# Optimization experiments

Hardware: AMD Instinct MI355X
Metric: run time of the kernel (lower is better)

The kernel has to match this reference:

```python
import jax, jax.numpy as jnp
import numpy as np

B, N, D = 2, 2048, 1024          # batch, seq (= wh*ww), model dim
H, HD = 16, 64                   # heads, head_dim (inner_dim = H*HD = D)
MLP = 4096                       # SwiGLU hidden dim
WSY, WSX = 16, 32                # ws_y = wh//2, ws_x = ww//2  (wh=32, ww=64)
EPS = float(jnp.finfo(jnp.float32).eps)  # torch RMSNorm default eps


def setup_inputs() -> dict:
    key = jax.random.key(0)
    ks = jax.random.split(key, 8)
    return {
        "x": jax.random.normal(ks[0], (B, N, D), jnp.float32),
        "t": jax.random.normal(ks[1], (B,), jnp.float32),
        "dt": jax.random.normal(ks[2], (B, D), jnp.float32),
        "w_qkv": (jax.random.normal(ks[3], (3 * H * HD, D), jnp.float32) * 0.02),
        "w_o": (jax.random.normal(ks[4], (D, H * HD), jnp.float32) * 0.02),
        "w1": (jax.random.normal(ks[5], (2 * MLP, D), jnp.float32) * 0.02),
        "w2": (jax.random.normal(ks[6], (D, MLP), jnp.float32) * 0.02),
        "g_attn": jnp.ones((D,), jnp.float32),  # RMSNorm weight (attn)
        "g_ff": jnp.ones((D,), jnp.float32),    # RMSNorm weight (ffn)
    }


def _rms(x, g):
    return x * jax.lax.rsqrt(jnp.mean(x * x, axis=-1, keepdims=True) + EPS) * g


def _win(x):
    # 'b h (wc_y wc_x ws_y ws_x) d' -> 'b h (wc_y ws_y wc_x ws_x) d'
    b, h, n, d = x.shape
    return x.reshape(b, h, 2, 2, WSY, WSX, d).transpose(0, 1, 2, 4, 3, 5, 6).reshape(b, h, n, d)


def _unwin(x):
    # inverse of _win
    b, h, n, d = x.shape
    return x.reshape(b, h, 2, WSY, 2, WSX, d).transpose(0, 1, 2, 4, 3, 5, 6).reshape(b, h, n, d)


def reference(x, t, dt, w_qkv, w_o, w1, w2, g_attn, g_ff):
    # ---- SPAttention (pre-norm); all-to-all is identity on 1 device ----
    h = _rms(x, g_attn)
    qkv = h @ w_qkv.T                              # [B,N,3*H*HD]
    q, k, v = jnp.split(qkv, 3, axis=-1)
    as_heads = lambda z: z.reshape(B, N, H, HD).transpose(0, 2, 1, 3)  # b h n d
    q, k, v = _win(as_heads(q)), _win(as_heads(k)), _win(as_heads(v))
    # NOTE: the source computes RoPE2D(q), RoPE2D(k) but discards the result;
    # attention consumes the UNROTATED seq_gathered_q/k/v. Faithful: no rotation.
    scale = 1.0 / jnp.sqrt(jnp.float32(HD))        # SDPA default scale
    s = jnp.einsum('bhqd,bhkd->bhqk', q, k) * scale
    a = jax.nn.softmax(s, axis=-1)
    o = jnp.einsum('bhqk,bhkd->bhqd', a, v)
    o = _unwin(o).transpose(0, 2, 1, 3).reshape(B, N, H * HD)
    x = x + o @ w_o.T                               # residual
    # ---- SwiGLU FeedForward (pre-norm) + residual ----
    hf = _rms(x, g_ff)
    gate, up = jnp.split(hf @ w1.T, 2, axis=-1)
    return x + (jax.nn.silu(gate) * up) @ w2.T
```

## Files before the change

### kernel.cpp

```cpp
#include <hip/hip_runtime.h>
#include <cstdint>
#include <cstddef>

typedef __attribute__((ext_vector_type(8)))  __bf16 bf16x8;
typedef __attribute__((ext_vector_type(4)))  __bf16 bf16x4;
typedef __attribute__((ext_vector_type(4)))  float  f32x4;
typedef __attribute__((ext_vector_type(16))) float  f32x16;
typedef __attribute__((ext_vector_type(4)))  uint32_t u32x4;

#define MFMA_BF16(a, b, c) __builtin_amdgcn_mfma_f32_16x16x32_bf16((a), (b), (c), 0, 0, 0)
#define MFMA32(a, b, c)    __builtin_amdgcn_mfma_f32_32x32x16_bf16((a), (b), (c), 0, 0, 0)

__device__ __forceinline__ void gload_lds16(const __bf16* src, __bf16* lds_dst) {
    __builtin_amdgcn_global_load_lds(
        (const __attribute__((address_space(1))) void*)(const_cast<__bf16*>(src)),
        (__attribute__((address_space(3))) void*)(lds_dst), 16, 0, 0);
}

__device__ __forceinline__ uint32_t pack2(float a, float b) {
    uint16_t ua = __builtin_bit_cast(uint16_t, (__bf16)a);
    uint16_t ub = __builtin_bit_cast(uint16_t, (__bf16)b);
    return (uint32_t)ua | ((uint32_t)ub << 16);
}

__global__ __launch_bounds__(256) void cvt_kernel(const float* __restrict__ src,
                                                  __bf16* __restrict__ dst) {
    int i = blockIdx.x * 256 + threadIdx.x;
    float4 v = reinterpret_cast<const float4*>(src)[i];
    bf16x4 o;
    o[0] = (__bf16)v.x; o[1] = (__bf16)v.y; o[2] = (__bf16)v.z; o[3] = (__bf16)v.w;
    reinterpret_cast<bf16x4*>(dst)[i] = o;
}

__global__ __launch_bounds__(256) void rmsnorm_kernel(const float* __restrict__ x,
                                                      const float* __restrict__ g,
                                                      __bf16* __restrict__ out) {
    const int row = blockIdx.x;
    const int t = threadIdx.x;
    float4 v = reinterpret_cast<const float4*>(x + (size_t)row * 1024)[t];
    float ss = v.x * v.x + v.y * v.y + v.z * v.z + v.w * v.w;
#pragma unroll
    for (int m = 1; m < 64; m <<= 1) ss += __shfl_xor(ss, m);
    __shared__ float sred[4];
    if ((t & 63) == 0) sred[t >> 6] = ss;
    __syncthreads();
    float tot = sred[0] + sred[1] + sred[2] + sred[3];
    float rs = rsqrtf(tot * (1.0f / 1024.0f) + 1.1920928955078125e-07f);
    float4 gv = reinterpret_cast<const float4*>(g)[t];
    bf16x4 o;
    o[0] = (__bf16)(v.x * rs * gv.x);
    o[1] = (__bf16)(v.y * rs * gv.y);
    o[2] = (__bf16)(v.z * rs * gv.z);
    o[3] = (__bf16)(v.w * rs * gv.w);
    *reinterpret_cast<bf16x4*>(out + (size_t)row * 1024 + t * 4) = o;
}

template <int MODE>
__global__ __launch_bounds__(256) void gemm_nt(const __bf16* __restrict__ A, int lda,
                                               const __bf16* __restrict__ B, int ldb,
                                               __bf16* __restrict__ outb,
                                               float* __restrict__ outf,
                                               const float* __restrict__ resid,
                                               int K, int ldo) {
    __shared__ __attribute__((aligned(16))) __bf16 As[128 * 64];
    __shared__ __attribute__((aligned(16))) __bf16 Bs[128 * 64];
    const int t = threadIdx.x;
    const int lane = t & 63;
    const int wid = t >> 6;
    const int bm = blockIdx.x, bn = blockIdx.y;
    const int wm = (wid >> 1) * 64, wn = (wid & 1) * 64;
    f32x4 acc[4][4] = {};

    for (int kt = 0; kt < K; kt += 64) {
        __syncthreads();
#pragma unroll
        for (int i = 0; i < 4; ++i) {
            int L = i * 256 + t;
            int r = L >> 3, s = L & 7;
            int c = s ^ (r & 7);
            const __bf16* sa = A + (size_t)(bm * 128 + r) * lda + kt + c * 8;
            gload_lds16(sa, As + L * 8);
            int rb = bn * 128 + r;
            int srow = (MODE == 2) ? ((rb >> 1) + ((rb & 1) << 12)) : rb;
            const __bf16* sb = B + (size_t)srow * ldb + kt + c * 8;
            gload_lds16(sb, Bs + L * 8);
        }
        __syncthreads();
#pragma unroll
        for (int ks = 0; ks < 2; ++ks) {
            bf16x8 af[4], bfr[4];
#pragma unroll
            for (int mi = 0; mi < 4; ++mi) {
                int r = wm + mi * 16 + (lane & 15);
                int slot = (ks * 4 + (lane >> 4)) ^ (r & 7);
                af[mi] = *reinterpret_cast<const bf16x8*>(As + r * 64 + slot * 8);
            }
#pragma unroll
            for (int ni = 0; ni < 4; ++ni) {
                int r = wn + ni * 16 + (lane & 15);
                int slot = (ks * 4 + (lane >> 4)) ^ (r & 7);
                bfr[ni] = *reinterpret_cast<const bf16x8*>(Bs + r * 64 + slot * 8);
            }
#pragma unroll
            for (int mi = 0; mi < 4; ++mi)
#pragma unroll
                for (int ni = 0; ni < 4; ++ni)
                    acc[mi][ni] = MFMA_BF16(af[mi], bfr[ni], acc[mi][ni]);
        }
    }
    const int row0 = bm * 128 + wm + ((lane >> 4) << 2);
    const int col0 = bn * 128 + wn + (lane & 15);
#pragma unroll
    for (int mi = 0; mi < 4; ++mi)
#pragma unroll
        for (int ni = 0; ni < 4; ++ni)
#pragma unroll
            for (int r2 = 0; r2 < 4; ++r2) {
                int row = row0 + mi * 16 + r2;
                int col = col0 + ni * 16;
                float v = acc[mi][ni][r2];
                if (MODE == 0) {
                    outb[(size_t)row * ldo + col] = (__bf16)v;
                } else if (MODE == 1) {
                    size_t idx = (size_t)row * ldo + col;
                    outf[idx] = v + resid[idx];
                } else {
                    float pv = __shfl_xor(v, 1);
                    if (!(lane & 1)) {
                        float sg = v / (1.0f + __expf(-v));
                        outb[(size_t)row * ldo + (col >> 1)] = (__bf16)(sg * pv);
                    }
                }
            }
}

__global__ __launch_bounds__(256) void vtrans_kernel(const __bf16* __restrict__ qkv,
                                                     __bf16* __restrict__ vt) {
    __shared__ __bf16 T[64][68];
    const int t = threadIdx.x;
    const int bh = blockIdx.y, b = bh >> 4, h = bh & 15;
    const int n0 = blockIdx.x * 64;
    const __bf16* vp = qkv + (size_t)b * 2048 * 3072 + 2048 + h * 64;
#pragma unroll
    for (int i = 0; i < 2; ++i) {
        int r = i * 32 + (t >> 3), c = t & 7;
        bf16x8 v = *reinterpret_cast<const bf16x8*>(vp + (size_t)(n0 + r) * 3072 + c * 8);
#pragma unroll
        for (int j = 0; j < 8; ++j) T[c * 8 + j][r] = v[j];
    }
    __syncthreads();
#pragma unroll
    for (int i = 0; i < 2; ++i) {
        int hd = i * 32 + (t >> 3), c = t & 7;
        bf16x8 v;
#pragma unroll
        for (int j = 0; j < 8; ++j) v[j] = T[hd][c * 8 + j];
        *reinterpret_cast<bf16x8*>(vt + ((size_t)bh * 64 + hd) * 2048 + n0 + c * 8) = v;
    }
}

__global__ __launch_bounds__(256) void attn_kernel(const __bf16* __restrict__ qkv,
                                                   const __bf16* __restrict__ vt,
                                                   __bf16* __restrict__ o) {
    __shared__ __attribute__((aligned(16))) __bf16 Ks[2][64 * 64];
    __shared__ __attribute__((aligned(16))) __bf16 Vs[2][64 * 64];
    const int t = threadIdx.x;
    const int lane = t & 63;
    const int w = t >> 6;
    const int hi = lane >> 5;
    const int l31 = lane & 31;
    const int bh = blockIdx.y;
    const int b = bh >> 4, h = bh & 15;
    const __bf16* qp = qkv + (size_t)b * 2048 * 3072 + h * 64;
    const __bf16* kp = qp + 1024;
    const __bf16* vtp = vt + (size_t)bh * 64 * 2048;
    const int q0 = blockIdx.x * 128 + w * 32;

    const float SC = 0.18033688011112042f;
    bf16x8 qf[4];
#pragma unroll
    for (int s = 0; s < 4; ++s) {
        bf16x8 raw = *reinterpret_cast<const bf16x8*>(
            qp + (size_t)(q0 + l31) * 3072 + s * 16 + hi * 8);
        bf16x8 sc;
#pragma unroll
        for (int j = 0; j < 8; ++j) sc[j] = (__bf16)((float)raw[j] * SC);
        qf[s] = sc;
    }

    f32x16 oa[2] = {};
    float m_run = -INFINITY, l_run = 0.0f;

    auto stage = [&](int buf, int kt) {
#pragma unroll
        for (int i = 0; i < 2; ++i) {
            int L = i * 256 + t;
            int r = L >> 3, s = L & 7;
            int c = s ^ (r & 7);
            gload_lds16(kp + (size_t)(kt + r) * 3072 + c * 8, &Ks[buf][L * 8]);
            gload_lds16(vtp + (size_t)r * 2048 + kt + c * 8, &Vs[buf][L * 8]);
        }
    };
    stage(0, 0);
    __syncthreads();

    for (int kt = 0; kt < 2048; kt += 64) {
        const int buf = (kt >> 6) & 1;
        if (kt + 64 < 2048) stage(buf ^ 1, kt + 64);

        f32x16 st[2] = {};
#pragma unroll
        for (int s = 0; s < 4; ++s) {
#pragma unroll
            for (int mb = 0; mb < 2; ++mb) {
                int r = mb * 32 + l31;
                int sl = (s * 2 + hi) ^ (r & 7);
                bf16x8 kf = *reinterpret_cast<const bf16x8*>(&Ks[buf][r * 64 + sl * 8]);
                st[mb] = MFMA32(kf, qf[s], st[mb]);
            }
        }
        float mt = -INFINITY;
#pragma unroll
        for (int mb = 0; mb < 2; ++mb)
#pragma unroll
            for (int r = 0; r < 16; ++r) mt = fmaxf(mt, st[mb][r]);
        mt = fmaxf(mt, __shfl_xor(mt, 32));
        const float m_new = fmaxf(m_run, mt);
        const float alpha = exp2f(m_run - m_new);
        float ps = 0.0f;
#pragma unroll
        for (int mb = 0; mb < 2; ++mb)
#pragma unroll
            for (int r = 0; r < 16; ++r) {
                float p = exp2f(st[mb][r] - m_new);
                st[mb][r] = p;
                ps += p;
            }
        ps += __shfl_xor(ps, 32);
        l_run = l_run * alpha + ps;
        m_run = m_new;

#pragma unroll
        for (int r = 0; r < 16; ++r) {
            float av = __shfl(alpha, (r & 3) + 8 * (r >> 2) + 4 * hi);
            oa[0][r] *= av;
            oa[1][r] *= av;
        }

        uint32_t pk[16], qk[16];
#pragma unroll
        for (int mb = 0; mb < 2; ++mb)
#pragma unroll
            for (int i2 = 0; i2 < 8; ++i2)
                pk[mb * 8 + i2] = pack2(st[mb][2 * i2], st[mb][2 * i2 + 1]);
#pragma unroll
        for (int i2 = 0; i2 < 16; ++i2)
            qk[i2] = (uint32_t)__shfl_xor((int)pk[i2], 32);

#pragma unroll
        for (int s2 = 0; s2 < 4; ++s2) {
            int mb = s2 >> 1, sl2 = s2 & 1;
            u32x4 fv;
            if (hi == 0) {
                fv[0] = pk[mb * 8 + 4 * sl2 + 0]; fv[1] = pk[mb * 8 + 4 * sl2 + 1];
                fv[2] = qk[mb * 8 + 4 * sl2 + 0]; fv[3] = qk[mb * 8 + 4 * sl2 + 1];
            } else {
                fv[0] = qk[mb * 8 + 4 * sl2 + 2]; fv[1] = qk[mb * 8 + 4 * sl2 + 3];
                fv[2] = pk[mb * 8 + 4 * sl2 + 2]; fv[3] = pk[mb * 8 + 4 * sl2 + 3];
            }
            bf16x8 pa = __builtin_bit_cast(bf16x8, fv);
#pragma unroll
            for (int nb = 0; nb < 2; ++nb) {
                int rv = nb * 32 + l31;
                int sl = (s2 * 2 + hi) ^ (rv & 7);
                bf16x8 vf = *reinterpret_cast<const bf16x8*>(&Vs[buf][rv * 64 + sl * 8]);
                oa[nb] = MFMA32(pa, vf, oa[nb]);
            }
        }
        __syncthreads();
    }

#pragma unroll
    for (int r = 0; r < 16; ++r) {
        int crow = (r & 3) + 8 * (r >> 2) + 4 * hi;
        float lv = __shfl(l_run, crow);
        float inv = 1.0f / lv;
        int row = q0 + crow;
        size_t base = ((size_t)b * 2048 + row) * 1024 + h * 64 + l31;
        o[base]      = (__bf16)(oa[0][r] * inv);
        o[base + 32] = (__bf16)(oa[1][r] * inv);
    }
}

extern "C" void kernel_launch(void* const* d_in, const int* in_sizes, int n_in,
                              void* d_out, int out_size, void* d_ws, size_t ws_size,
                              hipStream_t stream) {
    const float* x      = (const float*)d_in[0];
    const float* w_qkv  = (const float*)d_in[3];
    const float* w_o    = (const float*)d_in[4];
    const float* w1     = (const float*)d_in[5];
    const float* w2     = (const float*)d_in[6];
    const float* g_attn = (const float*)d_in[7];
    const float* g_ff   = (const float*)d_in[8];
    float* out = (float*)d_out;

    char* ws = (char*)d_ws;
    size_t off = 0;
    auto alloc = [&](size_t bytes) -> void* {
        void* p = ws + off;
        off += (bytes + 255) & ~(size_t)255;
        return p;
    };
    __bf16* wqkv_b = (__bf16*)alloc((size_t)3072 * 1024 * 2);
    __bf16* wo_b   = (__bf16*)alloc((size_t)1024 * 1024 * 2);
    __bf16* w1_b   = (__bf16*)alloc((size_t)8192 * 1024 * 2);
    __bf16* w2_b   = (__bf16*)alloc((size_t)1024 * 4096 * 2);
    __bf16* h_b    = (__bf16*)alloc((size_t)4096 * 1024 * 2);
    __bf16* qkv_b  = (__bf16*)alloc((size_t)4096 * 3072 * 2);
    __bf16* o_b    = (__bf16*)alloc((size_t)4096 * 1024 * 2);
    float*  x2     = (float*)alloc((size_t)4096 * 1024 * 4);
    __bf16* vt_b   = (__bf16*)alloc((size_t)32 * 64 * 2048 * 2);
    __bf16* act_b  = qkv_b;

    cvt_kernel<<<3072, 256, 0, stream>>>(w_qkv, wqkv_b);
    cvt_kernel<<<1024, 256, 0, stream>>>(w_o, wo_b);
    cvt_kernel<<<8192, 256, 0, stream>>>(w1, w1_b);
    cvt_kernel<<<4096, 256, 0, stream>>>(w2, w2_b);

    rmsnorm_kernel<<<4096, 256, 0, stream>>>(x, g_attn, h_b);
    gemm_nt<0><<<dim3(32, 24), 256, 0, stream>>>(h_b, 1024, wqkv_b, 1024,
                                                 qkv_b, nullptr, nullptr, 1024, 3072);
    vtrans_kernel<<<dim3(32, 32), 256, 0, stream>>>(qkv_b, vt_b);
    attn_kernel<<<dim3(16, 32), 256, 0, stream>>>(qkv_b, vt_b, o_b);
    gemm_nt<1><<<dim3(32, 8), 256, 0, stream>>>(o_b, 1024, wo_b, 1024,
                                                nullptr, x2, x, 1024, 1024);
    rmsnorm_kernel<<<4096, 256, 0, stream>>>(x2, g_ff, h_b);
    gemm_nt<2><<<dim3(32, 64), 256, 0, stream>>>(h_b, 1024, w1_b, 1024,
                                                 act_b, nullptr, nullptr, 1024, 4096);
    gemm_nt<1><<<dim3(32, 8), 256, 0, stream>>>(act_b, 4096, w2_b, 4096,
                                                nullptr, out, x2, 4096, 1024);
}
```

Measured before the change: 354.3 us.

## Widen attention KV tiles, add lazy rescale, permlane swap, narrower GEMM N-tiles

The attention kernel now stages 128 keys per iteration and processes them as two 64-key halves. It skips the output rescale unless the running max grows by more than 8 (lazy rescaling) and builds P fragments with permlane32_swap in place of 16 shuffles. The V tile uses a 16-way swizzle for its wider layout. Separately, the GEMM is templated on N-tile width, and the two N=1024 output GEMMs use 64-wide tiles so they launch twice as many blocks on the 256-CU device. These changes cut sync and shuffle overhead and exp/rescale work and improve GEMM occupancy, at the cost of more LDS use in attention and less reuse per block in the narrower GEMMs.

Measured after the change: 320.2 us. 1.11x faster.

```diff
diff --git a/kernel.cpp b/kernel.cpp
--- a/kernel.cpp
+++ b/kernel.cpp
@@ -6,6 +6,7 @@
 typedef __attribute__((ext_vector_type(4)))  __bf16 bf16x4;
 typedef __attribute__((ext_vector_type(4)))  float  f32x4;
 typedef __attribute__((ext_vector_type(16))) float  f32x16;
+typedef __attribute__((ext_vector_type(2)))  uint32_t u32x2;
 typedef __attribute__((ext_vector_type(4)))  uint32_t u32x4;
 
 #define MFMA_BF16(a, b, c) __builtin_amdgcn_mfma_f32_16x16x32_bf16((a), (b), (c), 0, 0, 0)
@@ -55,21 +56,22 @@
     *reinterpret_cast<bf16x4*>(out + (size_t)row * 1024 + t * 4) = o;
 }
 
-template <int MODE>
+template <int MODE, int NB>
 __global__ __launch_bounds__(256) void gemm_nt(const __bf16* __restrict__ A, int lda,
                                                const __bf16* __restrict__ B, int ldb,
                                                __bf16* __restrict__ outb,
                                                float* __restrict__ outf,
                                                const float* __restrict__ resid,
                                                int K, int ldo) {
+    constexpr int BN = NB * 32;
     __shared__ __attribute__((aligned(16))) __bf16 As[128 * 64];
-    __shared__ __attribute__((aligned(16))) __bf16 Bs[128 * 64];
+    __shared__ __attribute__((aligned(16))) __bf16 Bs[BN * 64];
     const int t = threadIdx.x;
     const int lane = t & 63;
     const int wid = t >> 6;
     const int bm = blockIdx.x, bn = blockIdx.y;
-    const int wm = (wid >> 1) * 64, wn = (wid & 1) * 64;
-    f32x4 acc[4][4] = {};
+    const int wm = (wid >> 1) * 64, wn = (wid & 1) * (NB * 16);
+    f32x4 acc[4][NB] = {};
 
     for (int kt = 0; kt < K; kt += 64) {
         __syncthreads();
@@ -78,17 +80,21 @@
             int L = i * 256 + t;
             int r = L >> 3, s = L & 7;
             int c = s ^ (r & 7);
-            const __bf16* sa = A + (size_t)(bm * 128 + r) * lda + kt + c * 8;
-            gload_lds16(sa, As + L * 8);
-            int rb = bn * 128 + r;
+            gload_lds16(A + (size_t)(bm * 128 + r) * lda + kt + c * 8, As + L * 8);
+        }
+#pragma unroll
+        for (int i = 0; i < NB; ++i) {
+            int L = i * 256 + t;
+            int r = L >> 3, s = L & 7;
+            int c = s ^ (r & 7);
+            int rb = bn * BN + r;
             int srow = (MODE == 2) ? ((rb >> 1) + ((rb & 1) << 12)) : rb;
-            const __bf16* sb = B + (size_t)srow * ldb + kt + c * 8;
-            gload_lds16(sb, Bs + L * 8);
+            gload_lds16(B + (size_t)srow * ldb + kt + c * 8, Bs + L * 8);
         }
         __syncthreads();
 #pragma unroll
         for (int ks = 0; ks < 2; ++ks) {
-            bf16x8 af[4], bfr[4];
+            bf16x8 af[4], bfr[NB];
 #pragma unroll
             for (int mi = 0; mi < 4; ++mi) {
                 int r = wm + mi * 16 + (lane & 15);
@@ -96,7 +102,7 @@
                 af[mi] = *reinterpret_cast<const bf16x8*>(As + r * 64 + slot * 8);
             }
 #pragma unroll
-            for (int ni = 0; ni < 4; ++ni) {
+            for (int ni = 0; ni < NB; ++ni) {
                 int r = wn + ni * 16 + (lane & 15);
                 int slot = (ks * 4 + (lane >> 4)) ^ (r & 7);
                 bfr[ni] = *reinterpret_cast<const bf16x8*>(Bs + r * 64 + slot * 8);
@@ -104,16 +110,16 @@
 #pragma unroll
             for (int mi = 0; mi < 4; ++mi)
 #pragma unroll
-                for (int ni = 0; ni < 4; ++ni)
+                for (int ni = 0; ni < NB; ++ni)
                     acc[mi][ni] = MFMA_BF16(af[mi], bfr[ni], acc[mi][ni]);
         }
     }
     const int row0 = bm * 128 + wm + ((lane >> 4) << 2);
-    const int col0 = bn * 128 + wn + (lane & 15);
+    const int col0 = bn * BN + wn + (lane & 15);
 #pragma unroll
     for (int mi = 0; mi < 4; ++mi)
 #pragma unroll
-        for (int ni = 0; ni < 4; ++ni)
+        for (int ni = 0; ni < NB; ++ni)
 #pragma unroll
             for (int r2 = 0; r2 < 4; ++r2) {
                 int row = row0 + mi * 16 + r2;
@@ -162,8 +168,8 @@
 __global__ __launch_bounds__(256) void attn_kernel(const __bf16* __restrict__ qkv,
                                                    const __bf16* __restrict__ vt,
                                                    __bf16* __restrict__ o) {
-    __shared__ __attribute__((aligned(16))) __bf16 Ks[2][64 * 64];
-    __shared__ __attribute__((aligned(16))) __bf16 Vs[2][64 * 64];
+    __shared__ __attribute__((aligned(16))) __bf16 Ks[2][128 * 64];
+    __shared__ __attribute__((aligned(16))) __bf16 Vs[2][64 * 128];
     const int t = threadIdx.x;
     const int lane = t & 63;
     const int w = t >> 6;
@@ -193,88 +199,93 @@
 
     auto stage = [&](int buf, int kt) {
 #pragma unroll
-        for (int i = 0; i < 2; ++i) {
+        for (int i = 0; i < 4; ++i) {
             int L = i * 256 + t;
             int r = L >> 3, s = L & 7;
             int c = s ^ (r & 7);
             gload_lds16(kp + (size_t)(kt + r) * 3072 + c * 8, &Ks[buf][L * 8]);
+        }
+#pragma unroll
+        for (int i = 0; i < 4; ++i) {
+            int L = i * 256 + t;
+            int r = L >> 4, s = L & 15;
+            int c = s ^ (r & 15);
             gload_lds16(vtp + (size_t)r * 2048 + kt + c * 8, &Vs[buf][L * 8]);
         }
     };
     stage(0, 0);
     __syncthreads();
 
-    for (int kt = 0; kt < 2048; kt += 64) {
-        const int buf = (kt >> 6) & 1;
-        if (kt + 64 < 2048) stage(buf ^ 1, kt + 64);
-
-        f32x16 st[2] = {};
-#pragma unroll
-        for (int s = 0; s < 4; ++s) {
-#pragma unroll
-            for (int mb = 0; mb < 2; ++mb) {
-                int r = mb * 32 + l31;
-                int sl = (s * 2 + hi) ^ (r & 7);
-                bf16x8 kf = *reinterpret_cast<const bf16x8*>(&Ks[buf][r * 64 + sl * 8]);
-                st[mb] = MFMA32(kf, qf[s], st[mb]);
-            }
-        }
-        float mt = -INFINITY;
-#pragma unroll
-        for (int mb = 0; mb < 2; ++mb)
-#pragma unroll
-            for (int r = 0; r < 16; ++r) mt = fmaxf(mt, st[mb][r]);
-        mt = fmaxf(mt, __shfl_xor(mt, 32));
-        const float m_new = fmaxf(m_run, mt);
-        const float alpha = exp2f(m_run - m_new);
-        float ps = 0.0f;
-#pragma unroll
-        for (int mb = 0; mb < 2; ++mb)
-#pragma unroll
-            for (int r = 0; r < 16; ++r) {
-                float p = exp2f(st[mb][r] - m_new);
-                st[mb][r] = p;
-                ps += p;
-            }
-        ps += __shfl_xor(ps, 32);
-        l_run = l_run * alpha + ps;
-        m_run = m_new;
-
-#pragma unroll
-        for (int r = 0; r < 16; ++r) {
-            float av = __shfl(alpha, (r & 3) + 8 * (r >> 2) + 4 * hi);
-            oa[0][r] *= av;
-            oa[1][r] *= av;
-        }
-
-        uint32_t pk[16], qk[16];
-#pragma unroll
-        for (int mb = 0; mb < 2; ++mb)
-#pragma unroll
-            for (int i2 = 0; i2 < 8; ++i2)
-                pk[mb * 8 + i2] = pack2(st[mb][2 * i2], st[mb][2 * i2 + 1]);
-#pragma unroll
-        for (int i2 = 0; i2 < 16; ++i2)
-            qk[i2] = (uint32_t)__shfl_xor((int)pk[i2], 32);
-
-#pragma unroll
-        for (int s2 = 0; s2 < 4; ++s2) {
-            int mb = s2 >> 1, sl2 = s2 & 1;
-            u32x4 fv;
-            if (hi == 0) {
-                fv[0] = pk[mb * 8 + 4 * sl2 + 0]; fv[1] = pk[mb * 8 + 4 * sl2 + 1];
-                fv[2] = qk[mb * 8 + 4 * sl2 + 0]; fv[3] = qk[mb * 8 + 4 * sl2 + 1];
-            } else {
-                fv[0] = qk[mb * 8 + 4 * sl2 + 2]; fv[1] = qk[mb * 8 + 4 * sl2 + 3];
-                fv[2] = pk[mb * 8 + 4 * sl2 + 2]; fv[3] = pk[mb * 8 + 4 * sl2 + 3];
-            }
-            bf16x8 pa = __builtin_bit_cast(bf16x8, fv);
-#pragma unroll
-            for (int nb = 0; nb < 2; ++nb) {
-                int rv = nb * 32 + l31;
-                int sl = (s2 * 2 + hi) ^ (rv & 7);
-                bf16x8 vf = *reinterpret_cast<const bf16x8*>(&Vs[buf][rv * 64 + sl * 8]);
-                oa[nb] = MFMA32(pa, vf, oa[nb]);
+    for (int kt = 0; kt < 2048; kt += 128) {
+        const int buf = (kt >> 7) & 1;
+        if (kt + 128 < 2048) stage(buf ^ 1, kt + 128);
+
+#pragma unroll
+        for (int h2 = 0; h2 < 2; ++h2) {
+            f32x16 st[2] = {};
+#pragma unroll
+            for (int s = 0; s < 4; ++s) {
+#pragma unroll
+                for (int mb = 0; mb < 2; ++mb) {
+                    int r = h2 * 64 + mb * 32 + l31;
+                    int sl = (s * 2 + hi) ^ (r & 7);
+                    bf16x8 kf = *reinterpret_cast<const bf16x8*>(&Ks[buf][r * 64 + sl * 8]);
+                    st[mb] = MFMA32(kf, qf[s], st[mb]);
+                }
+            }
+            float mt = -INFINITY;
+#pragma unroll
+            for (int mb = 0; mb < 2; ++mb)
+#pragma unroll
+                for (int r = 0; r < 16; ++r) mt = fmaxf(mt, st[mb][r]);
+            mt = fmaxf(mt, __shfl_xor(mt, 32));
+            if (__any(mt > m_run + 8.0f)) {
+                float m_new = fmaxf(m_run, mt);
+                float alpha = exp2f(m_run - m_new);
+#pragma unroll
+                for (int r = 0; r < 16; ++r) {
+                    float av = __shfl(alpha, (r & 3) + 8 * (r >> 2) + 4 * hi);
+                    oa[0][r] *= av;
+                    oa[1][r] *= av;
+                }
+                l_run *= alpha;
+                m_run = m_new;
+            }
+            float ps = 0.0f;
+#pragma unroll
+            for (int mb = 0; mb < 2; ++mb)
+#pragma unroll
+                for (int r = 0; r < 16; ++r) {
+                    float p = exp2f(st[mb][r] - m_run);
+                    st[mb][r] = p;
+                    ps += p;
+                }
+            ps += __shfl_xor(ps, 32);
+            l_run += ps;
+
+            uint32_t pk[16];
+#pragma unroll
+            for (int mb = 0; mb < 2; ++mb)
+#pragma unroll
+                for (int i2 = 0; i2 < 8; ++i2)
+                    pk[mb * 8 + i2] = pack2(st[mb][2 * i2], st[mb][2 * i2 + 1]);
+
+#pragma unroll
+            for (int s2 = 0; s2 < 4; ++s2) {
+                const int I0 = (s2 >> 1) * 8 + (s2 & 1) * 4;
+                u32x2 w02 = __builtin_amdgcn_permlane32_swap(pk[I0], pk[I0 + 2], false, false);
+                u32x2 w13 = __builtin_amdgcn_permlane32_swap(pk[I0 + 1], pk[I0 + 3], false, false);
+                u32x4 fv;
+                fv[0] = w02[0]; fv[1] = w13[0]; fv[2] = w02[1]; fv[3] = w13[1];
+                bf16x8 pa = __builtin_bit_cast(bf16x8, fv);
+#pragma unroll
+                for (int nb = 0; nb < 2; ++nb) {
+                    int rv = nb * 32 + l31;
+                    int ch = h2 * 8 + s2 * 2 + hi;
+                    int sl = ch ^ (rv & 15);
+                    bf16x8 vf = *reinterpret_cast<const bf16x8*>(&Vs[buf][rv * 128 + sl * 8]);
+                    oa[nb] = MFMA32(pa, vf, oa[nb]);
+                }
             }
         }
         __syncthreads();
@@ -328,15 +339,15 @@
     cvt_kernel<<<4096, 256, 0, stream>>>(w2, w2_b);
 
     rmsnorm_kernel<<<4096, 256, 0, stream>>>(x, g_attn, h_b);
-    gemm_nt<0><<<dim3(32, 24), 256, 0, stream>>>(h_b, 1024, wqkv_b, 1024,
-                                                 qkv_b, nullptr, nullptr, 1024, 3072);
+    gemm_nt<0, 4><<<dim3(32, 24), 256, 0, stream>>>(h_b, 1024, wqkv_b, 1024,
+                                                    qkv_b, nullptr, nullptr, 1024, 3072);
     vtrans_kernel<<<dim3(32, 32), 256, 0, stream>>>(qkv_b, vt_b);
     attn_kernel<<<dim3(16, 32), 256, 0, stream>>>(qkv_b, vt_b, o_b);
-    gemm_nt<1><<<dim3(32, 8), 256, 0, stream>>>(o_b, 1024, wo_b, 1024,
-                                                nullptr, x2, x, 1024, 1024);
+    gemm_nt<1, 2><<<dim3(32, 16), 256, 0, stream>>>(o_b, 1024, wo_b, 1024,
+                                                    nullptr, x2, x, 1024, 1024);
     rmsnorm_kernel<<<4096, 256, 0, stream>>>(x2, g_ff, h_b);
-    gemm_nt<2><<<dim3(32, 64), 256, 0, stream>>>(h_b, 1024, w1_b, 1024,
-                                                 act_b, nullptr, nullptr, 1024, 4096);
-    gemm_nt<1><<<dim3(32, 8), 256, 0, stream>>>(act_b, 4096, w2_b, 4096,
-                                                nullptr, out, x2, 4096, 1024);
-}
+    gemm_nt<2, 4><<<dim3(32, 64), 256, 0, stream>>>(h_b, 1024, w1_b, 1024,
+                                                    act_b, nullptr, nullptr, 1024, 4096);
+    gemm_nt<1, 2><<<dim3(32, 16), 256, 0, stream>>>(act_b, 4096, w2_b, 4096,
+                                                    nullptr, out, x2, 4096, 1024);
+}
```
